# Kernel optimization log

Measured on AMD Instinct MI355X. Metric: run time of the kernel, lower is better.

The kernel has to match this reference:

```python
import jax, jax.numpy as jnp
import numpy as np

THETA = 10000.0
B, S, D, H = 2, 2048, 1024, 16
DK = D // H


def setup_inputs() -> dict:
    key = jax.random.key(0)
    k1, k2, k3 = jax.random.split(key, 3)
    x = jax.random.normal(k1, (B, S, D), jnp.float32)
    # trunc_normal init approximated by scaled normal (std = 2/(d_k+d_model))
    weight = jax.random.normal(k2, (3, H, DK, D), jnp.float32) * (2.0 / (DK + D))
    wo_weight = jax.random.normal(k3, (D, H * DK), jnp.float32) * (2.0 / (2 * D))
    token_positions = jnp.arange(S, dtype=jnp.int32)
    return {"x": x, "token_positions": token_positions, "weight": weight, "wo_weight": wo_weight}


def _rope(x, cos, sin):
    # x: (..., seq, d_k); rotate interleaved pairs
    x1 = jnp.stack((-x[..., 1::2], x[..., ::2]), axis=-1).reshape(x.shape)
    return x * cos + x1 * sin


def _masked_softmax(scores, mask):
    # matches reference: exp(x - rowmax over ALL entries), zero masked, normalize, zero again
    e = jnp.exp(scores - jnp.max(scores, axis=-1, keepdims=True))
    e = jnp.where(mask, e, 0.0)
    a = e / jnp.sum(e, axis=-1, keepdims=True)
    return jnp.where(mask, a, 0.0)


def reference(x, token_positions, weight, wo_weight):
    dk = weight.shape[2]
    seq_len = x.shape[-2]
    # fused QKV projection: (b, 3, h, s, dk)
    qkv = jnp.einsum('bsd,qhkd->bqhsk', x, weight)
    # RoPE tables from token positions
    pos = token_positions.astype(jnp.float32)[:, None]          # (s, 1)
    kidx = jnp.arange(1, dk // 2 + 1, dtype=jnp.float32)[None]  # (1, dk/2)
    theta = pos / (THETA ** ((2.0 * kidx - 2.0) / dk))          # (s, dk/2)
    cos = jnp.repeat(jnp.cos(theta), 2, axis=-1)                # (s, dk)
    sin = jnp.repeat(jnp.sin(theta), 2, axis=-1)
    q = _rope(qkv[:, 0], cos, sin)   # (b, h, s, dk)
    k = _rope(qkv[:, 1], cos, sin)
    v = qkv[:, 2]
    scores = jnp.einsum('bhqd,bhkd->bhqk', q, k) / jnp.sqrt(jnp.float32(dk))
    mask = jnp.tril(jnp.ones((seq_len, seq_len), dtype=bool))
    att = _masked_softmax(scores, mask)
    out = jnp.einsum('bhqk,bhkd->bhqd', att, v)                 # (b, h, s, dv)
    out = jnp.transpose(out, (0, 2, 1, 3)).reshape(*x.shape[:-1], -1)  # (b, s, h*dv)
    return jnp.einsum('bsi,oi->bso', out, wo_weight)
```

## Files before the change

### kernel.cpp

```cpp
#include <hip/hip_runtime.h>
#include <hip/hip_bf16.h>
#include <math.h>

#define B_   2
#define S_   2048
#define D_   1024
#define H_   16
#define DK_  64
#define NQKV 3072
#define M_   (B_ * S_)

typedef unsigned short u16;
typedef unsigned int   u32;
typedef __attribute__((ext_vector_type(8))) short short8;
typedef __attribute__((ext_vector_type(4))) float f32x4;
typedef __attribute__((ext_vector_type(4))) u16   u16x4;

typedef const __attribute__((address_space(1))) void* gvptr;
typedef __attribute__((address_space(3))) void* lvptr;

#define QSCALE 0.18033688011f

#if __has_builtin(__builtin_amdgcn_exp2f)
#define EXP2F(x) __builtin_amdgcn_exp2f(x)
#else
#define EXP2F(x) __expf(0.69314718056f * (x))
#endif

__device__ __forceinline__ u16 f2bf(float f) {
  union { float f; u32 u; } v; v.f = f;
  u32 r = v.u + 0x7FFF + ((v.u >> 16) & 1);
  return (u16)(r >> 16);
}
__device__ __forceinline__ float bf2f(u16 h) {
  union { u32 u; float f; } v; v.u = ((u32)h) << 16;
  return v.f;
}
__device__ __forceinline__ u32 cvtpk_bf16(float lo, float hi) {
  u32 r;
  asm("v_cvt_pk_bf16_f32 %0, %1, %2" : "=v"(r) : "v"(lo), "v"(hi));
  return r;
}

#define MEMFENCE() asm volatile("" ::: "memory")
#define RAW_BARRIER() do { MEMFENCE(); __builtin_amdgcn_s_barrier(); MEMFENCE(); } while (0)

#define SWZ(r) ((((r) & 7) ^ ((((r) >> 3) & 1) << 2)))

__global__ void rope_cs_kernel(const int* __restrict__ pos,
                               float2* __restrict__ cs) {
  int idx = blockIdx.x * 256 + threadIdx.x;
  int i = idx & 31;
  int s = idx >> 5;
  double p = (double)pos[s];
  double t = p * pow(10000.0, -(double)i / 32.0);
  cs[idx] = make_float2((float)cos(t), (float)sin(t));
}

#define N4X (M_ * D_ / 4)
#define N4W (NQKV * D_ / 4)
#define N4WO (D_ * D_ / 4)
__global__ void cvt_all_kernel(const float* __restrict__ x,
                               const float* __restrict__ w,
                               const float* __restrict__ wo,
                               u16* __restrict__ dst) {
  int i = blockIdx.x * 256 + threadIdx.x;
  float4 v;
  if (i < N4X)            v = ((const float4*)x)[i];
  else if (i < N4X + N4W) v = ((const float4*)w)[i - N4X];
  else                    v = ((const float4*)wo)[i - (N4X + N4W)];
  u16x4 o;
  o[0] = f2bf(v.x); o[1] = f2bf(v.y); o[2] = f2bf(v.z); o[3] = f2bf(v.w);
  ((u16x4*)dst)[i] = o;
}

template<bool OUT_BF16, bool ROPE>
__global__ __launch_bounds__(256) void gemm_nt_mfma(const u16* __restrict__ A,
                                                    const u16* __restrict__ Bm,
                                                    void* __restrict__ Cout,
                                                    const float2* __restrict__ cstab,
                                                    int Nd, int Kd) {
  __shared__ u16 As[2][128 * 64];
  __shared__ u16 Bs[2][128 * 64];
  const int t  = threadIdx.x;
  const int w  = t >> 6, l = t & 63;
  const int g  = l >> 4, ln = l & 15;
  const int wm = w >> 1, wn = w & 1;
  const int m0 = blockIdx.y * 128, n0 = blockIdx.x * 128;

  const int sr = t >> 3;
  auto stage = [&](int buf, int k0) {
#pragma unroll
    for (int p = 0; p < 4; ++p) {
      int r = p * 32 + sr;
      int sx = (t & 7) ^ (r & 7);
      __builtin_amdgcn_global_load_lds(
          (gvptr)(A + (size_t)(m0 + r) * Kd + k0 + sx * 8),
          (lvptr)(&As[buf][(p * 256 + w * 64) * 8]), 16, 0, 0);
      __builtin_amdgcn_global_load_lds(
          (gvptr)(Bm + (size_t)(n0 + r) * Kd + k0 + sx * 8),
          (lvptr)(&Bs[buf][(p * 256 + w * 64) * 8]), 16, 0, 0);
    }
  };

  const f32x4 vzero = {0.f, 0.f, 0.f, 0.f};
  f32x4 acc[4][4];
#pragma unroll
  for (int i = 0; i < 4; ++i)
#pragma unroll
    for (int j = 0; j < 4; ++j) acc[i][j] = vzero;

  const int nkt = Kd >> 6;
  stage(0, 0);
  int cur = 0;
#pragma unroll 1
  for (int kt = 0; kt < nkt; ++kt) {
    if (kt + 1 < nkt) {
      stage(cur ^ 1, (kt + 1) * 64);
      asm volatile("s_waitcnt vmcnt(8)" ::: "memory");
    } else {
      asm volatile("s_waitcnt vmcnt(0)" ::: "memory");
    }
    RAW_BARRIER();

    __builtin_amdgcn_s_setprio(1);
#pragma unroll
    for (int ks = 0; ks < 2; ++ks) {
      short8 af[4], bf[4];
#pragma unroll
      for (int i = 0; i < 4; ++i) {
        int ra = wm * 64 + i * 16 + ln;
        af[i] = *(const short8*)&As[cur][ra * 64 + (((ks * 4 + g) ^ (ra & 7)) * 8)];
        int rb = wn * 64 + i * 16 + ln;
        bf[i] = *(const short8*)&Bs[cur][rb * 64 + (((ks * 4 + g) ^ (rb & 7)) * 8)];
      }
#pragma unroll
      for (int i = 0; i < 4; ++i)
#pragma unroll
        for (int j = 0; j < 4; ++j)
          acc[i][j] = __builtin_amdgcn_mfma_f32_16x16x32_bf16(af[i], bf[j], acc[i][j], 0, 0, 0);
    }
    __builtin_amdgcn_s_setprio(0);

    asm volatile("s_waitcnt lgkmcnt(0)" ::: "memory");
    RAW_BARRIER();
    cur ^= 1;
  }

  if (ROPE && n0 < 2048) {
#pragma unroll
    for (int i = 0; i < 4; ++i)
#pragma unroll
      for (int r = 0; r < 4; ++r) {
        int rowi = m0 + wm * 64 + i * 16 + g * 4 + r;
        int srow = rowi & (S_ - 1);
#pragma unroll
        for (int j = 0; j < 4; ++j) {
          int dk = j * 16 + ln;
          float2 cs = cstab[srow * 32 + (dk >> 1)];
          float v = acc[i][j][r];
          float p = __shfl_xor(v, 1);
          float sn = (ln & 1) ? cs.y : -cs.y;
          float rot = fmaf(p, sn, v * cs.x);
          ((u16*)Cout)[(size_t)rowi * Nd + n0 + wn * 64 + j * 16 + ln] = f2bf(rot);
        }
      }
  } else {
#pragma unroll
    for (int i = 0; i < 4; ++i)
#pragma unroll
      for (int j = 0; j < 4; ++j)
#pragma unroll
        for (int r = 0; r < 4; ++r) {
          size_t row = (size_t)(m0 + wm * 64 + i * 16 + g * 4 + r);
          size_t col = (size_t)(n0 + wn * 64 + j * 16 + ln);
          if (OUT_BF16) ((u16*)Cout)[row * Nd + col] = f2bf(acc[i][j][r]);
          else          ((float*)Cout)[row * Nd + col] = acc[i][j][r];
        }
  }
}

__global__ __launch_bounds__(256) void gemm_small_mfma(const u16* __restrict__ A,
                                                       const u16* __restrict__ Bm,
                                                       float* __restrict__ C,
                                                       int Nd, int Kd) {
  __shared__ u16 As[2][64 * 64];
  __shared__ u16 Bs[2][64 * 64];
  const int t  = threadIdx.x;
  const int w  = t >> 6, l = t & 63;
  const int g  = l >> 4, ln = l & 15;
  const int wm = w >> 1, wn = w & 1;
  const int m0 = blockIdx.y * 64, n0 = blockIdx.x * 64;

  auto stage = [&](int buf, int k0) {
#pragma unroll
    for (int p = 0; p < 2; ++p) {
      int c = p * 256 + t;
      int r = c >> 3;
      int sx = (c & 7) ^ (r & 7);
      __builtin_amdgcn_global_load_lds(
          (gvptr)(A + (size_t)(m0 + r) * Kd + k0 + sx * 8),
          (lvptr)(&As[buf][(p * 256 + w * 64) * 8]), 16, 0, 0);
      __builtin_amdgcn_global_load_lds(
          (gvptr)(Bm + (size_t)(n0 + r) * Kd + k0 + sx * 8),
          (lvptr)(&Bs[buf][(p * 256 + w * 64) * 8]), 16, 0, 0);
    }
  };

  const f32x4 vzero = {0.f, 0.f, 0.f, 0.f};
  f32x4 acc[2][2];
#pragma unroll
  for (int i = 0; i < 2; ++i)
#pragma unroll
    for (int j = 0; j < 2; ++j) acc[i][j] = vzero;

  const int nkt = Kd >> 6;
  stage(0, 0);
  int cur = 0;
#pragma unroll 1
  for (int kt = 0; kt < nkt; ++kt) {
    if (kt + 1 < nkt) {
      stage(cur ^ 1, (kt + 1) * 64);
      asm volatile("s_waitcnt vmcnt(4)" ::: "memory");
    } else {
      asm volatile("s_waitcnt vmcnt(0)" ::: "memory");
    }
    RAW_BARRIER();

    __builtin_amdgcn_s_setprio(1);
#pragma unroll
    for (int ks = 0; ks < 2; ++ks) {
      short8 af[2], bf[2];
#pragma unroll
      for (int i = 0; i < 2; ++i) {
        int ra = wm * 32 + i * 16 + ln;
        af[i] = *(const short8*)&As[cur][ra * 64 + (((ks * 4 + g) ^ (ra & 7)) * 8)];
        int rb = wn * 32 + i * 16 + ln;
        bf[i] = *(const short8*)&Bs[cur][rb * 64 + (((ks * 4 + g) ^ (rb & 7)) * 8)];
      }
#pragma unroll
      for (int i = 0; i < 2; ++i)
#pragma unroll
        for (int j = 0; j < 2; ++j)
          acc[i][j] = __builtin_amdgcn_mfma_f32_16x16x32_bf16(af[i], bf[j], acc[i][j], 0, 0, 0);
    }
    __builtin_amdgcn_s_setprio(0);

    asm volatile("s_waitcnt lgkmcnt(0)" ::: "memory");
    RAW_BARRIER();
    cur ^= 1;
  }

#pragma unroll
  for (int i = 0; i < 2; ++i)
#pragma unroll
    for (int j = 0; j < 2; ++j)
#pragma unroll
      for (int r = 0; r < 4; ++r)
        C[(size_t)(m0 + wm * 32 + i * 16 + g * 4 + r) * Nd + n0 + wn * 32 + j * 16 + ln]
            = acc[i][j][r];
}

__global__ __launch_bounds__(256) void v_transpose_kernel(const u16* __restrict__ qkvb,
                                                          u16* __restrict__ Vt) {
  __shared__ u16 tile[64][72];
  const int t = threadIdx.x;
  const int s0 = blockIdx.x * 64, h = blockIdx.y, b = blockIdx.z;
  {
    int r = t >> 2, cs = (t & 3) * 16;
    const u16* src = qkvb + (size_t)(b * S_ + s0 + r) * NQKV + 2048 + h * 64 + cs;
    u16 v[16];
    *(uint4*)&v[0] = *(const uint4*)src;
    *(uint4*)&v[8] = *(const uint4*)(src + 8);
#pragma unroll
    for (int j = 0; j < 16; ++j) tile[cs + j][r] = v[j];
  }
  __syncthreads();
  {
    int d = t >> 2, ss = (t & 3) * 16;
    u16 o[16];
#pragma unroll
    for (int j = 0; j < 16; ++j) o[j] = tile[d][ss + j];
    u16* dst = Vt + ((size_t)(b * H_ + h) * 64 + d) * S_ + s0 + ss;
    *(uint4*)&dst[0] = *(uint4*)&o[0];
    *(uint4*)&dst[8] = *(uint4*)&o[8];
  }
}

__global__ __launch_bounds__(512) void attn_mfma(const u16* __restrict__ qkvb,
                                                 const u16* __restrict__ Vt,
                                                 u16* __restrict__ attb) {
  __shared__ u16 Ks[2][128 * 64];
  __shared__ u16 Vs[2][64 * 128];
  const int t = threadIdx.x;
  const int w = t >> 6, l = t & 63;
  const int g = l >> 4, ln = l & 15;
  const int bx = blockIdx.x, h = blockIdx.y, b = blockIdx.z;
  const size_t bS = (size_t)b * S_;
  const u16* Kbase = qkvb + bS * NQKV + D_ + h * 64;
  const u16* Vbase = Vt + (size_t)(b * H_ + h) * 64 * S_;

  auto stage = [&](int buf, int k0) {
#pragma unroll
    for (int p = 0; p < 2; ++p) {
      int ck = p * 512 + t;
      int rk = ck >> 3, sk = (ck & 7) ^ SWZ(rk);
      __builtin_amdgcn_global_load_lds(
          (gvptr)(Kbase + (size_t)(k0 + rk) * NQKV + sk * 8),
          (lvptr)(&Ks[buf][(p * 512 + w * 64) * 8]), 16, 0, 0);
      int cv = p * 512 + t;
      int rv = cv >> 4, sv = (cv & 15) ^ (rv & 15);
      __builtin_amdgcn_global_load_lds(
          (gvptr)(Vbase + (size_t)rv * S_ + k0 + sv * 8),
          (lvptr)(&Vs[buf][(p * 512 + w * 64) * 8]), 16, 0, 0);
    }
  };

  const f32x4 vzero = {0.f, 0.f, 0.f, 0.f};

  const int tqH = 15 - bx, tqL = bx;
  const int q0H = tqH * 128, q0L = tqL * 128;
  const int nt = 16 - bx;
  const int ntL = bx + 1;
  const int qgH = q0H + w * 16 + ln;
  const int qgL = q0L + w * 16 + ln;

  short8 qfH[2], qfL[2];
  {
    const u16* qr = qkvb + (bS + q0H + w * 16 + ln) * NQKV + h * 64;
    qfH[0] = *(const short8*)(qr + g * 8);
    qfH[1] = *(const short8*)(qr + 32 + g * 8);
    qr = qkvb + (bS + q0L + w * 16 + ln) * NQKV + h * 64;
    qfL[0] = *(const short8*)(qr + g * 8);
    qfL[1] = *(const short8*)(qr + 32 + g * 8);
#pragma unroll
    for (int kx = 0; kx < 2; ++kx)
#pragma unroll
      for (int e = 0; e < 8; ++e) {
        qfH[kx][e] = (short)f2bf(bf2f((u16)qfH[kx][e]) * QSCALE);
        qfL[kx][e] = (short)f2bf(bf2f((u16)qfL[kx][e]) * QSCALE);
      }
  }

  f32x4 oH[4], oL[4];
#pragma unroll
  for (int dt = 0; dt < 4; ++dt) { oH[dt] = vzero; oL[dt] = vzero; }
  float mH = -INFINITY, lH = 0.f, mL = -INFINITY, lL = 0.f;

  auto chain = [&](const short8* qf, f32x4* o, float& mrun, float& lrun,
                   int qg, bool maskTile, int k0, int cur) {
    f32x4 sacc[8];
#pragma unroll
    for (int st = 0; st < 8; ++st) sacc[st] = vzero;
    __builtin_amdgcn_s_setprio(1);
#pragma unroll
    for (int st = 0; st < 8; ++st) {
      const int pr = ((ln >> 2) << 3) + ((st & 1) << 2) + (ln & 3) + ((st >> 1) << 5);
#pragma unroll
      for (int ks = 0; ks < 2; ++ks) {
        short8 kf = *(const short8*)&Ks[cur][pr * 64 + (((ks * 4 + g) ^ SWZ(pr)) * 8)];
        sacc[st] = __builtin_amdgcn_mfma_f32_16x16x32_bf16(kf, qf[ks], sacc[st], 0, 0, 0);
      }
    }
    __builtin_amdgcn_s_setprio(0);

    float tmax = -INFINITY;
    if (maskTile) {
#pragma unroll
      for (int st = 0; st < 8; ++st)
#pragma unroll
        for (int r = 0; r < 4; ++r) {
          int key = k0 + g * 8 + ((st & 1) << 2) + r + ((st >> 1) << 5);
          if (key > qg) sacc[st][r] = -INFINITY;
          tmax = fmaxf(tmax, sacc[st][r]);
        }
    } else {
#pragma unroll
      for (int st = 0; st < 8; ++st)
#pragma unroll
        for (int r = 0; r < 4; ++r) tmax = fmaxf(tmax, sacc[st][r]);
    }
    tmax = fmaxf(tmax, __shfl_xor(tmax, 16));
    tmax = fmaxf(tmax, __shfl_xor(tmax, 32));
    float al = 1.f, mnew = mrun;
    if (!__all(tmax <= mrun + 8.0f)) {
      mnew = fmaxf(mrun, tmax);
      al = EXP2F(mrun - mnew);
#pragma unroll
      for (int r = 0; r < 4; ++r) {
        float srs = __shfl(al, g * 4 + r);
#pragma unroll
        for (int dt = 0; dt < 4; ++dt) o[dt][r] *= srs;
      }
    }
    float lsum = 0.f;
#pragma unroll
    for (int st = 0; st < 8; ++st)
#pragma unroll
      for (int r = 0; r < 4; ++r) {
        float pe = EXP2F(sacc[st][r] - mnew);
        sacc[st][r] = pe;
        lsum += pe;
      }
    lsum += __shfl_xor(lsum, 16);
    lsum += __shfl_xor(lsum, 32);
    lrun = lrun * al + lsum;
    mrun = mnew;

    union { u32 u[4]; short8 v; } pa[4];
#pragma unroll
    for (int ks = 0; ks < 4; ++ks) {
      pa[ks].u[0] = cvtpk_bf16(sacc[2 * ks][0], sacc[2 * ks][1]);
      pa[ks].u[1] = cvtpk_bf16(sacc[2 * ks][2], sacc[2 * ks][3]);
      pa[ks].u[2] = cvtpk_bf16(sacc[2 * ks + 1][0], sacc[2 * ks + 1][1]);
      pa[ks].u[3] = cvtpk_bf16(sacc[2 * ks + 1][2], sacc[2 * ks + 1][3]);
    }

    __builtin_amdgcn_s_setprio(1);
#pragma unroll
    for (int ks = 0; ks < 4; ++ks)
#pragma unroll
      for (int dt = 0; dt < 4; ++dt) {
        const int dr = dt * 16 + ln;
        short8 vf = *(const short8*)&Vs[cur][dr * 128 + (((ks * 4 + g) ^ (dr & 15)) * 8)];
        o[dt] = __builtin_amdgcn_mfma_f32_16x16x32_bf16(pa[ks].v, vf, o[dt], 0, 0, 0);
      }
    __builtin_amdgcn_s_setprio(0);
  };

  stage(0, 0);
  int cur = 0;
#pragma unroll 1
  for (int kt = 0; kt < nt; ++kt) {
    const int k0 = kt * 128;
    if (kt + 1 < nt) {
      stage(cur ^ 1, k0 + 128);
      asm volatile("s_waitcnt vmcnt(4)" ::: "memory");
    } else {
      asm volatile("s_waitcnt vmcnt(0)" ::: "memory");
    }
    RAW_BARRIER();

    chain(qfH, oH, mH, lH, qgH, kt == nt - 1, k0, cur);
    if (kt < ntL)
      chain(qfL, oL, mL, lL, qgL, kt == tqL, k0, cur);

    asm volatile("s_waitcnt lgkmcnt(0)" ::: "memory");
    RAW_BARRIER();
    cur ^= 1;
  }

  {
    float linv = 1.f / lH;
#pragma unroll
    for (int r = 0; r < 4; ++r) {
      float ir = __shfl(linv, g * 4 + r);
      size_t row = bS + q0H + w * 16 + g * 4 + r;
#pragma unroll
      for (int dt = 0; dt < 4; ++dt)
        attb[row * D_ + h * 64 + dt * 16 + ln] = f2bf(oH[dt][r] * ir);
    }
  }
  {
    float linv = 1.f / lL;
#pragma unroll
    for (int r = 0; r < 4; ++r) {
      float ir = __shfl(linv, g * 4 + r);
      size_t row = bS + q0L + w * 16 + g * 4 + r;
#pragma unroll
      for (int dt = 0; dt < 4; ++dt)
        attb[row * D_ + h * 64 + dt * 16 + ln] = f2bf(oL[dt][r] * ir);
    }
  }
}

extern "C" void kernel_launch(void* const* d_in, const int* in_sizes, int n_in,
                              void* d_out, int out_size, void* d_ws, size_t ws_size,
                              hipStream_t stream) {
  (void)in_sizes; (void)n_in; (void)out_size; (void)ws_size;
  const float* x   = (const float*)d_in[0];
  const int*   pos = (const int*)d_in[1];
  const float* w   = (const float*)d_in[2];
  const float* wo  = (const float*)d_in[3];
  float* out = (float*)d_out;

  u16* qkvb = (u16*)d_ws;
  u16* Vt   = qkvb + (size_t)M_ * NQKV;
  u16* attb = Vt + (size_t)B_ * H_ * 64 * S_;
  u16* xb   = attb + (size_t)M_ * D_;
  u16* wb   = xb + (size_t)M_ * D_;
  u16* wob  = wb + (size_t)NQKV * D_;
  float2* cstab = (float2*)(wob + (size_t)D_ * D_);

  rope_cs_kernel<<<(S_ * 32) / 256, 256, 0, stream>>>(pos, cstab);

  cvt_all_kernel<<<(N4X + N4W + N4WO) / 256, 256, 0, stream>>>(x, w, wo, xb);

  gemm_nt_mfma<true, true><<<dim3(NQKV / 128, M_ / 128), 256, 0, stream>>>(
      xb, wb, qkvb, cstab, NQKV, D_);

  v_transpose_kernel<<<dim3(S_ / 64, H_, B_), 256, 0, stream>>>(qkvb, Vt);

  attn_mfma<<<dim3(8, H_, B_), 512, 0, stream>>>(qkvb, Vt, attb);

  gemm_small_mfma<<<dim3(D_ / 64, M_ / 64), 256, 0, stream>>>(
      attb, wob, out, D_, D_);
}
```

Before: 189.3 us.

## Fuse RoPE table and V transpose into neighbouring kernels, single-buffer QKV GEMM

```diff
diff --git a/kernel.cpp b/kernel.cpp
--- a/kernel.cpp
+++ b/kernel.cpp
@@ -47,61 +47,49 @@
 
 #define SWZ(r) ((((r) & 7) ^ ((((r) >> 3) & 1) << 2)))
 
-__global__ void rope_cs_kernel(const int* __restrict__ pos,
-                               float2* __restrict__ cs) {
-  int idx = blockIdx.x * 256 + threadIdx.x;
-  int i = idx & 31;
-  int s = idx >> 5;
-  double p = (double)pos[s];
-  double t = p * pow(10000.0, -(double)i / 32.0);
-  cs[idx] = make_float2((float)cos(t), (float)sin(t));
-}
-
 #define N4X (M_ * D_ / 4)
 #define N4W (NQKV * D_ / 4)
 #define N4WO (D_ * D_ / 4)
+#define NCVT (N4X + N4W + N4WO)
 __global__ void cvt_all_kernel(const float* __restrict__ x,
                                const float* __restrict__ w,
                                const float* __restrict__ wo,
-                               u16* __restrict__ dst) {
+                               u16* __restrict__ dst,
+                               const int* __restrict__ pos,
+                               float2* __restrict__ cs) {
   int i = blockIdx.x * 256 + threadIdx.x;
-  float4 v;
-  if (i < N4X)            v = ((const float4*)x)[i];
-  else if (i < N4X + N4W) v = ((const float4*)w)[i - N4X];
-  else                    v = ((const float4*)wo)[i - (N4X + N4W)];
-  u16x4 o;
-  o[0] = f2bf(v.x); o[1] = f2bf(v.y); o[2] = f2bf(v.z); o[3] = f2bf(v.w);
-  ((u16x4*)dst)[i] = o;
-}
-
-template<bool OUT_BF16, bool ROPE>
-__global__ __launch_bounds__(256) void gemm_nt_mfma(const u16* __restrict__ A,
-                                                    const u16* __restrict__ Bm,
-                                                    void* __restrict__ Cout,
-                                                    const float2* __restrict__ cstab,
-                                                    int Nd, int Kd) {
-  __shared__ u16 As[2][128 * 64];
-  __shared__ u16 Bs[2][128 * 64];
+  if (i < NCVT) {
+    float4 v;
+    if (i < N4X)            v = ((const float4*)x)[i];
+    else if (i < N4X + N4W) v = ((const float4*)w)[i - N4X];
+    else                    v = ((const float4*)wo)[i - (N4X + N4W)];
+    u16x4 o;
+    o[0] = f2bf(v.x); o[1] = f2bf(v.y); o[2] = f2bf(v.z); o[3] = f2bf(v.w);
+    ((u16x4*)dst)[i] = o;
+  } else {
+    int idx = i - NCVT;
+    int fi = idx & 31;
+    int s = idx >> 5;
+    double p = (double)pos[s];
+    double t = p * pow(10000.0, -(double)fi / 32.0);
+    cs[idx] = make_float2((float)cos(t), (float)sin(t));
+  }
+}
+
+__global__ __launch_bounds__(256) void gemm_qkv_mfma(const u16* __restrict__ A,
+                                                     const u16* __restrict__ Bm,
+                                                     u16* __restrict__ qkvb,
+                                                     u16* __restrict__ Vt,
+                                                     const float2* __restrict__ cstab) {
+  __shared__ u16 lds[2 * 128 * 64];
+  u16* Asp = lds;
+  u16* Bsp = lds + 128 * 64;
   const int t  = threadIdx.x;
   const int w  = t >> 6, l = t & 63;
   const int g  = l >> 4, ln = l & 15;
   const int wm = w >> 1, wn = w & 1;
   const int m0 = blockIdx.y * 128, n0 = blockIdx.x * 128;
-
-  const int sr = t >> 3;
-  auto stage = [&](int buf, int k0) {
-#pragma unroll
-    for (int p = 0; p < 4; ++p) {
-      int r = p * 32 + sr;
-      int sx = (t & 7) ^ (r & 7);
-      __builtin_amdgcn_global_load_lds(
-          (gvptr)(A + (size_t)(m0 + r) * Kd + k0 + sx * 8),
-          (lvptr)(&As[buf][(p * 256 + w * 64) * 8]), 16, 0, 0);
-      __builtin_amdgcn_global_load_lds(
-          (gvptr)(Bm + (size_t)(n0 + r) * Kd + k0 + sx * 8),
-          (lvptr)(&Bs[buf][(p * 256 + w * 64) * 8]), 16, 0, 0);
-    }
-  };
+  const int Kd = D_, Nd = NQKV;
 
   const f32x4 vzero = {0.f, 0.f, 0.f, 0.f};
   f32x4 acc[4][4];
@@ -110,29 +98,30 @@
 #pragma unroll
     for (int j = 0; j < 4; ++j) acc[i][j] = vzero;
 
-  const int nkt = Kd >> 6;
-  stage(0, 0);
-  int cur = 0;
-#pragma unroll 1
-  for (int kt = 0; kt < nkt; ++kt) {
-    if (kt + 1 < nkt) {
-      stage(cur ^ 1, (kt + 1) * 64);
-      asm volatile("s_waitcnt vmcnt(8)" ::: "memory");
-    } else {
-      asm volatile("s_waitcnt vmcnt(0)" ::: "memory");
-    }
-    RAW_BARRIER();
-
-    __builtin_amdgcn_s_setprio(1);
+  for (int k0 = 0; k0 < Kd; k0 += 64) {
+    __syncthreads();
+#pragma unroll
+    for (int p = 0; p < 4; ++p) {
+      int c = p * 256 + t;
+      int r = c >> 3, sx = (c & 7) ^ (r & 7);
+      __builtin_amdgcn_global_load_lds(
+          (gvptr)(A + (size_t)(m0 + r) * Kd + k0 + sx * 8),
+          (lvptr)(&Asp[(p * 256 + w * 64) * 8]), 16, 0, 0);
+      __builtin_amdgcn_global_load_lds(
+          (gvptr)(Bm + (size_t)(n0 + r) * Kd + k0 + sx * 8),
+          (lvptr)(&Bsp[(p * 256 + w * 64) * 8]), 16, 0, 0);
+    }
+    __syncthreads();
+
 #pragma unroll
     for (int ks = 0; ks < 2; ++ks) {
       short8 af[4], bf[4];
 #pragma unroll
       for (int i = 0; i < 4; ++i) {
         int ra = wm * 64 + i * 16 + ln;
-        af[i] = *(const short8*)&As[cur][ra * 64 + (((ks * 4 + g) ^ (ra & 7)) * 8)];
+        af[i] = *(const short8*)&Asp[ra * 64 + (((ks * 4 + g) ^ (ra & 7)) * 8)];
         int rb = wn * 64 + i * 16 + ln;
-        bf[i] = *(const short8*)&Bs[cur][rb * 64 + (((ks * 4 + g) ^ (rb & 7)) * 8)];
+        bf[i] = *(const short8*)&Bsp[rb * 64 + (((ks * 4 + g) ^ (rb & 7)) * 8)];
       }
 #pragma unroll
       for (int i = 0; i < 4; ++i)
@@ -140,14 +129,9 @@
         for (int j = 0; j < 4; ++j)
           acc[i][j] = __builtin_amdgcn_mfma_f32_16x16x32_bf16(af[i], bf[j], acc[i][j], 0, 0, 0);
     }
-    __builtin_amdgcn_s_setprio(0);
-
-    asm volatile("s_waitcnt lgkmcnt(0)" ::: "memory");
-    RAW_BARRIER();
-    cur ^= 1;
-  }
-
-  if (ROPE && n0 < 2048) {
+  }
+
+  if (n0 < 2048) {
 #pragma unroll
     for (int i = 0; i < 4; ++i)
 #pragma unroll
@@ -162,21 +146,35 @@
           float p = __shfl_xor(v, 1);
           float sn = (ln & 1) ? cs.y : -cs.y;
           float rot = fmaf(p, sn, v * cs.x);
-          ((u16*)Cout)[(size_t)rowi * Nd + n0 + wn * 64 + j * 16 + ln] = f2bf(rot);
+          qkvb[(size_t)rowi * Nd + n0 + wn * 64 + j * 16 + ln] = f2bf(rot);
         }
       }
   } else {
+    __syncthreads();
+    u16* tr = lds;
 #pragma unroll
     for (int i = 0; i < 4; ++i)
 #pragma unroll
-      for (int j = 0; j < 4; ++j)
-#pragma unroll
-        for (int r = 0; r < 4; ++r) {
-          size_t row = (size_t)(m0 + wm * 64 + i * 16 + g * 4 + r);
-          size_t col = (size_t)(n0 + wn * 64 + j * 16 + ln);
-          if (OUT_BF16) ((u16*)Cout)[row * Nd + col] = f2bf(acc[i][j][r]);
-          else          ((float*)Cout)[row * Nd + col] = acc[i][j][r];
-        }
+      for (int j = 0; j < 4; ++j) {
+        int col = wn * 64 + j * 16 + ln;
+        int rowb = wm * 64 + i * 16 + g * 4;
+#pragma unroll
+        for (int r = 0; r < 4; ++r)
+          tr[col * 128 + ((rowb + r) ^ ((col & 7) << 3))] = f2bf(acc[i][j][r]);
+      }
+    __syncthreads();
+    {
+      int col = t >> 1, half = t & 1;
+      int hh = ((n0 - 2048) >> 6) + (col >> 6);
+      int dk = col & 63;
+      int bb = m0 >> 11, sb = m0 & 2047;
+      u16* dstp = Vt + ((size_t)(bb * H_ + hh) * 64 + dk) * S_ + sb + half * 64;
+      const u16* srcp = tr + col * 128 + half * 64;
+      int p7 = col & 7;
+#pragma unroll
+      for (int q = 0; q < 8; ++q)
+        *(uint4*)(dstp + q * 8) = *(const uint4*)(srcp + ((q ^ p7) * 8));
+    }
   }
 }
 
@@ -259,32 +257,6 @@
       for (int r = 0; r < 4; ++r)
         C[(size_t)(m0 + wm * 32 + i * 16 + g * 4 + r) * Nd + n0 + wn * 32 + j * 16 + ln]
             = acc[i][j][r];
-}
-
-__global__ __launch_bounds__(256) void v_transpose_kernel(const u16* __restrict__ qkvb,
-                                                          u16* __restrict__ Vt) {
-  __shared__ u16 tile[64][72];
-  const int t = threadIdx.x;
-  const int s0 = blockIdx.x * 64, h = blockIdx.y, b = blockIdx.z;
-  {
-    int r = t >> 2, cs = (t & 3) * 16;
-    const u16* src = qkvb + (size_t)(b * S_ + s0 + r) * NQKV + 2048 + h * 64 + cs;
-    u16 v[16];
-    *(uint4*)&v[0] = *(const uint4*)src;
-    *(uint4*)&v[8] = *(const uint4*)(src + 8);
-#pragma unroll
-    for (int j = 0; j < 16; ++j) tile[cs + j][r] = v[j];
-  }
-  __syncthreads();
-  {
-    int d = t >> 2, ss = (t & 3) * 16;
-    u16 o[16];
-#pragma unroll
-    for (int j = 0; j < 16; ++j) o[j] = tile[d][ss + j];
-    u16* dst = Vt + ((size_t)(b * H_ + h) * 64 + d) * S_ + s0 + ss;
-    *(uint4*)&dst[0] = *(uint4*)&o[0];
-    *(uint4*)&dst[8] = *(uint4*)&o[8];
-  }
 }
 
 __global__ __launch_bounds__(512) void attn_mfma(const u16* __restrict__ qkvb,
@@ -492,14 +464,10 @@
   u16* wob  = wb + (size_t)NQKV * D_;
   float2* cstab = (float2*)(wob + (size_t)D_ * D_);
 
-  rope_cs_kernel<<<(S_ * 32) / 256, 256, 0, stream>>>(pos, cstab);
-
-  cvt_all_kernel<<<(N4X + N4W + N4WO) / 256, 256, 0, stream>>>(x, w, wo, xb);
-
-  gemm_nt_mfma<true, true><<<dim3(NQKV / 128, M_ / 128), 256, 0, stream>>>(
-      xb, wb, qkvb, cstab, NQKV, D_);
-
-  v_transpose_kernel<<<dim3(S_ / 64, H_, B_), 256, 0, stream>>>(qkvb, Vt);
+  cvt_all_kernel<<<NCVT / 256 + 256, 256, 0, stream>>>(x, w, wo, xb, pos, cstab);
+
+  gemm_qkv_mfma<<<dim3(NQKV / 128, M_ / 128), 256, 0, stream>>>(
+      xb, wb, qkvb, Vt, cstab);
 
   attn_mfma<<<dim3(8, H_, B_), 512, 0, stream>>>(qkvb, Vt, attb);
 
```

After: 187.8 us. About the same (-0.8%).
